# Optimization experiments

Hardware: AMD Instinct MI355X
Metric: run time of the kernel (lower is better)

## Reference

```python
import jax, jax.numpy as jnp
import numpy as np

B, N, C = 4, 8192, 128
NPOINT, NSAMPLE = 2048, 32
RADIUS = 0.1
EPS = 1e-5  # BatchNorm eps (eval mode with running stats)


def setup_inputs() -> dict:
    key = jax.random.key(0)
    k1, k2, k3 = jax.random.split(key, 3)
    return {
        "points_coor": jax.random.uniform(k1, (B, 3, N), dtype=jnp.float32),
        "points_fea": jax.random.normal(k2, (B, C, N), dtype=jnp.float32),
        "W": jax.random.normal(k3, (2 * C, C + 3), dtype=jnp.float32) * 0.05,
        "b": jnp.zeros((2 * C,), jnp.float32),
        "gamma": jnp.ones((2 * C,), jnp.float32),
        "beta": jnp.zeros((2 * C,), jnp.float32),
        "bn_mean": jnp.zeros((2 * C,), jnp.float32),
        "bn_var": jnp.ones((2 * C,), jnp.float32),
    }


def _fps_single(xyz):
    """Farthest point sampling for one cloud. xyz: (N,3) -> (NPOINT,) int32.
    Deterministic start at index 0 (torch version starts at a random index)."""
    n = xyz.shape[0]

    def body(carry, _):
        dist, farthest = carry
        centroid = xyz[farthest]                      # (3,)
        d = jnp.sum((xyz - centroid) ** 2, axis=-1)   # (N,)
        dist = jnp.minimum(dist, d)
        nxt = jnp.argmax(dist).astype(jnp.int32)
        return (dist, nxt), farthest

    init = (jnp.full((n,), 1e10, xyz.dtype), jnp.int32(0))
    (_, _), idx = jax.lax.scan(body, init, None, length=NPOINT)
    return idx


def _gather(points, idx):
    # points: (B,N,D), idx: (B,S,K) -> (B,S,K,D)
    return jax.vmap(lambda p, i: p[i])(points, idx)


def reference(points_coor, points_fea, W, b, gamma, beta, bn_mean, bn_var):
    coor = points_coor.transpose(0, 2, 1)  # (B,N,3)
    fea = points_fea.transpose(0, 2, 1)    # (B,N,C)

    # S: farthest point sampling
    fps_idx = jax.vmap(_fps_single)(coor)                              # (B,S)
    new_coor = jnp.take_along_axis(coor, fps_idx[:, :, None], axis=1)  # (B,S,3)

    # G: hybrid knn/ball query -- k nearest, out-of-radius replaced by nearest
    sq = (jnp.sum(new_coor ** 2, -1)[:, :, None]
          + jnp.sum(coor ** 2, -1)[:, None, :]
          - 2.0 * jnp.einsum('bsd,bnd->bsn', new_coor, coor))           # (B,S,N)
    neg_d, idx = jax.lax.top_k(-sq, NSAMPLE)                            # k smallest
    d = -neg_d
    group_idx = jnp.where(d > RADIUS ** 2, idx[:, :, 0:1], idx)         # (B,S,K)

    g_coor = (_gather(coor, group_idx) - new_coor[:, :, None, :]) / RADIUS  # (B,S,K,3)
    g_fea = _gather(fea, group_idx)                                         # (B,S,K,C)
    g = jnp.concatenate([g_fea, g_coor], axis=-1)                           # (B,S,K,C+3)

    # P: shared 1x1 conv + BN(eval) + ReLU, then max-pool over neighbors
    h = jnp.einsum('bskc,dc->bskd', g, W) + b
    h = gamma * (h - bn_mean) * jax.lax.rsqrt(bn_var + EPS) + beta
    h = jax.nn.relu(h)
    new_fea = jnp.max(h, axis=2)  # (B,S,2C)

    return new_coor.transpose(0, 2, 1), new_fea.transpose(0, 2, 1)
```

## Files before the change

kernel.cpp:

```cpp
#include <hip/hip_runtime.h>
#include <stdint.h>


typedef unsigned short u16;
typedef unsigned long long u64;
typedef __bf16 bf16x8 __attribute__((ext_vector_type(8)));
typedef float f32x4 __attribute__((ext_vector_type(4)));
typedef float f32x2 __attribute__((ext_vector_type(2)));

#define NB 4
#define NPTS 8192
#define CH 128
#define SPTS 2048
#define KN 32
#define CINP 160

__device__ __forceinline__ u16 f2b(float f) {
    unsigned x = __float_as_uint(f);
    unsigned r = (x + 0x7fffu + ((x >> 16) & 1u)) >> 16;
    return (u16)r;
}
__device__ __forceinline__ u64 umin64(u64 a, u64 b) { return a < b ? a : b; }

template <int CTRL>
__device__ __forceinline__ u64 dpp_max64(u64 k) {
    unsigned lo = (unsigned)k, hi = (unsigned)(k >> 32);
    unsigned mlo = (unsigned)__builtin_amdgcn_update_dpp((int)lo, (int)lo, CTRL, 0xF, 0xF, false);
    unsigned mhi = (unsigned)__builtin_amdgcn_update_dpp((int)hi, (int)hi, CTRL, 0xF, 0xF, false);
    u64 m = ((u64)mhi << 32) | mlo;
    return m > k ? m : k;
}
template <int CTRL>
__device__ __forceinline__ unsigned dpp_maxu(unsigned v) {
    unsigned mv = (unsigned)__builtin_amdgcn_update_dpp((int)v, (int)v, CTRL, 0xF, 0xF, false);
    return mv > v ? mv : v;
}

__global__ __launch_bounds__(256) void ktrans(const float* __restrict__ fea,
                                              u16* __restrict__ feaT) {
    __shared__ u16 T[128][130];
    int blk = blockIdx.x;
    int b = blk >> 6, nt = blk & 63;
    int n0 = nt * 128;
    int t = threadIdx.x;
#pragma unroll 4
    for (int it = 0; it < 64; ++it) {
        int idx = it * 256 + t;
        int c = idx >> 7, nl = idx & 127;
        T[nl][c] = f2b(fea[((size_t)(b * CH + c)) * NPTS + n0 + nl]);
    }
    __syncthreads();
#pragma unroll 4
    for (int it = 0; it < 64; ++it) {
        int idx = it * 256 + t;
        int nl = idx >> 7, c = idx & 127;
        feaT[((size_t)(b * NPTS + n0 + nl)) * CH + c] = T[nl][c];
    }
}

__global__ __launch_bounds__(256) void kmisc(const float* __restrict__ coor,
                                             const float* __restrict__ W,
                                             float* __restrict__ pp,
                                             u16* __restrict__ Wpad) {
    int gid = blockIdx.x * 256 + threadIdx.x;
    if (blockIdx.x < 128) {
        int n = gid & 8191, b = gid >> 13;
        const float* cb = coor + b * 3 * NPTS;
        float x = cb[n], y = cb[NPTS + n], z = cb[2 * NPTS + n];
        pp[gid] = __fadd_rn(__fadd_rn(__fmul_rn(x, x), __fmul_rn(y, y)),
                            __fmul_rn(z, z));
    } else {
        int i = gid - 128 * 256;
        if (i < 256 * CINP) {
            int d = i / CINP, k = i - d * CINP;
            Wpad[i] = (k < 131) ? f2b(W[d * 131 + k]) : (u16)0;
        }
    }
}

__global__ __launch_bounds__(256) void ksort(const float* __restrict__ coor,
                                             float* __restrict__ sxg,
                                             float* __restrict__ syg,
                                             float* __restrict__ szg,
                                             int* __restrict__ sog) {
    __shared__ int hist[16], base[16];
    int b = blockIdx.x, tid = threadIdx.x;
    const float* cb = coor + b * 3 * NPTS;
    if (tid < 16) hist[tid] = 0;
    __syncthreads();
    int bins[32];
#pragma unroll 4
    for (int i = 0; i < 32; ++i) {
        int n = tid * 32 + i;
        float x = cb[n], y = cb[NPTS + n];
        int bx = min(3, (int)(x * 4.0f));
        int by = min(3, (int)(y * 4.0f));
        int bin = by * 4 + bx;
        bins[i] = bin;
        atomicAdd(&hist[bin], 1);
    }
    __syncthreads();
    if (tid == 0) {
        int acc = 0;
        for (int k2 = 0; k2 < 16; ++k2) { base[k2] = acc; acc += hist[k2]; hist[k2] = 0; }
    }
    __syncthreads();
#pragma unroll 4
    for (int i = 0; i < 32; ++i) {
        int n = tid * 32 + i;
        int bin = bins[i];
        int pos = base[bin] + atomicAdd(&hist[bin], 1);
        sxg[b * NPTS + pos] = cb[n];
        syg[b * NPTS + pos] = cb[NPTS + n];
        szg[b * NPTS + pos] = cb[2 * NPTS + n];
        sog[b * NPTS + pos] = n;
    }
}

__global__ __launch_bounds__(1024) void kfps(const float* __restrict__ sxg,
                                             const float* __restrict__ syg,
                                             const float* __restrict__ szg,
                                             const int* __restrict__ sog,
                                             int* __restrict__ fpsIdx,
                                             float* __restrict__ outCoor) {
    __shared__ float4 sp[NPTS];
    __shared__ unsigned sWin[SPTS];
    __shared__ u64 sAtom[4];
    __shared__ int slot0s;
    int tid = threadIdx.x;
    int b = blockIdx.x;
    int lane = tid & 63;
    const float* gx = sxg + b * NPTS;
    const float* gy = syg + b * NPTS;
    const float* gz = szg + b * NPTS;
    const int* go = sog + b * NPTS;
    f32x2 X2[4], Y2[4], Z2[4], D2[4];
    unsigned PK[8];
    int n0 = tid * 8;
    if (tid < 4) sAtom[tid] = 0;
#pragma unroll
    for (int j = 0; j < 8; ++j) {
        float x = gx[n0 + j], y = gy[n0 + j], z = gz[n0 + j];
        sp[n0 + j] = make_float4(x, y, z, 0.0f);
        X2[j >> 1][j & 1] = x; Y2[j >> 1][j & 1] = y; Z2[j >> 1][j & 1] = z;
        D2[j >> 1][j & 1] = 1e10f;
        int oi = go[n0 + j];
        PK[j] = ((unsigned)oi << 16) | (unsigned)(n0 + j);
        if (oi == 0) slot0s = n0 + j;
    }
    float lox = X2[0][0], hix = lox, loy = Y2[0][0], hiy = loy, loz = Z2[0][0], hiz = loz;
#pragma unroll
    for (int j = 1; j < 8; ++j) {
        float x = X2[j >> 1][j & 1], y = Y2[j >> 1][j & 1], z = Z2[j >> 1][j & 1];
        lox = fminf(lox, x); hix = fmaxf(hix, x);
        loy = fminf(loy, y); hiy = fmaxf(hiy, y);
        loz = fminf(loz, z); hiz = fmaxf(hiz, z);
    }
#pragma unroll
    for (int off = 32; off > 0; off >>= 1) {
        lox = fminf(lox, __shfl_xor(lox, off)); hix = fmaxf(hix, __shfl_xor(hix, off));
        loy = fminf(loy, __shfl_xor(loy, off)); hiy = fmaxf(hiy, __shfl_xor(hiy, off));
        loz = fminf(loz, __shfl_xor(loz, off)); hiz = fmaxf(hiz, __shfl_xor(hiz, off));
    }
    __syncthreads();
    int far = slot0s;
    if (tid == 0) sWin[0] = (unsigned)slot0s;
    float wMaxF = 3.4e38f;
    u64 cachedKey = 1;
    for (int t = 1; t < SPTS; ++t) {
        float4 c = sp[far];
        float fx = c.x, fy = c.y, fz = c.z;
        float ddx = fmaxf(0.0f, fmaxf(lox - fx, fx - hix));
        float ddy = fmaxf(0.0f, fmaxf(loy - fy, fy - hiy));
        float ddz = fmaxf(0.0f, fmaxf(loz - fz, fz - hiz));
        float dmin2 = ddx * ddx + ddy * ddy + ddz * ddz;
        if (!(dmin2 * 0.9995f >= wMaxF)) {
            {
#pragma clang fp contract(off)
                f32x2 fx2 = {fx, fx}, fy2 = {fy, fy}, fz2 = {fz, fz};
#pragma unroll
                for (int i = 0; i < 4; ++i) {
                    f32x2 dx = X2[i] - fx2;
                    f32x2 dy = Y2[i] - fy2;
                    f32x2 dz = Z2[i] - fz2;
                    f32x2 s = (dx * dx + dy * dy) + dz * dz;
                    D2[i][0] = fminf(D2[i][0], s[0]);
                    D2[i][1] = fminf(D2[i][1], s[1]);
                }
            }
            float m01 = fmaxf(D2[0][0], D2[0][1]), m23 = fmaxf(D2[1][0], D2[1][1]);
            float m45 = fmaxf(D2[2][0], D2[2][1]), m67 = fmaxf(D2[3][0], D2[3][1]);
            float m = fmaxf(fmaxf(m01, m23), fmaxf(m45, m67));
            unsigned sel = 0xFFFFFFFFu;
#pragma unroll
            for (int j = 0; j < 8; ++j) {
                float dj = D2[j >> 1][j & 1];
                sel = (dj == m) ? (sel < PK[j] ? sel : PK[j]) : sel;
            }
            unsigned mbits = __float_as_uint(m);
            unsigned r = mbits;
            r = dpp_maxu<0xB1>(r);
            r = dpp_maxu<0x4E>(r);
            r = dpp_maxu<0x141>(r);
            r = dpp_maxu<0x140>(r);
            r = dpp_maxu<0x142>(r);
            r = dpp_maxu<0x143>(r);
            unsigned wmaxb = (unsigned)__builtin_amdgcn_readlane((int)r, 63);
            u64 ball = __ballot(mbits == wmaxb);
            unsigned wpk;
            if (__popcll(ball) == 1) {
                int l = __ffsll(ball) - 1;
                wpk = (unsigned)__builtin_amdgcn_readlane((int)sel, l);
            } else {
                u64 kk = (mbits == wmaxb) ? (((u64)wmaxb << 32) | (unsigned)~sel) : 0ull;
                kk = dpp_max64<0xB1>(kk);
                kk = dpp_max64<0x4E>(kk);
                kk = dpp_max64<0x141>(kk);
                kk = dpp_max64<0x140>(kk);
                kk = dpp_max64<0x142>(kk);
                kk = dpp_max64<0x143>(kk);
                unsigned lo = (unsigned)__builtin_amdgcn_readlane((int)(unsigned)kk, 63);
                wpk = ~lo;
            }
            cachedKey = ((u64)wmaxb << 32) | (unsigned)~wpk;
            wMaxF = __uint_as_float(wmaxb);
        }
        if (lane == 63) atomicMax(&sAtom[t & 3], cachedKey);
        if (tid == 0) sAtom[(t + 1) & 3] = 0;
        __syncthreads();
        u64 wk = sAtom[t & 3];
        unsigned pk = ~(unsigned)wk;
        far = (int)(pk & 0xFFFFu);
        if (tid == 0) sWin[t] = pk;
    }
    __syncthreads();
    for (int i = tid; i < SPTS; i += 1024) {
        unsigned pk = sWin[i];
        int slot = (int)(pk & 0xFFFFu);
        float4 c = sp[slot];
        fpsIdx[b * SPTS + i] = (int)(pk >> 16);
        float* oc = outCoor + b * 3 * SPTS + i;
        oc[0] = c.x; oc[SPTS] = c.y; oc[2 * SPTS] = c.z;
    }
}

__global__ __launch_bounds__(256) void kgroup(const float* __restrict__ coor,
                                              const float* __restrict__ pp,
                                              const int* __restrict__ fpsIdx,
                                              int* __restrict__ gidxOut) {
    __shared__ u64 buf[4][256];
    __shared__ int cnt[4];
    int tid = threadIdx.x;
    int wv = tid >> 6, lane = tid & 63;
    if (tid < 4) cnt[tid] = 0;
    __syncthreads();
    int row = blockIdx.x * 4 + wv;
    int b = row >> 11, s = row & 2047;
    const float* cb = coor + b * 3 * NPTS;
    int n0 = fpsIdx[b * SPTS + s];
    float cx = cb[n0], cy = cb[NPTS + n0], cz = cb[2 * NPTS + n0];
    float cc = __fadd_rn(__fadd_rn(__fmul_rn(cx, cx), __fmul_rn(cy, cy)),
                         __fmul_rn(cz, cz));
    const float* ppb = pp + b * NPTS;
    u64 mk = ~0ull;
    for (int n = lane; n < NPTS; n += 64) {
        float x = cb[n], y = cb[NPTS + n], z = cb[2 * NPTS + n];
        float dot = __fmaf_rn(cz, z, __fmaf_rn(cy, y, __fmul_rn(cx, x)));
        float sq = __fsub_rn(__fadd_rn(cc, ppb[n]), __fmul_rn(2.0f, dot));
        unsigned ub = __float_as_uint(sq);
        ub ^= (ub >> 31) ? 0xFFFFFFFFu : 0x80000000u;
        u64 key = ((u64)ub << 32) | (unsigned)n;
        mk = umin64(mk, key);
        if (sq <= 0.01f) {
            int p = atomicAdd(&cnt[wv], 1);
            if (p < 256) buf[wv][p] = key;
        }
    }
#pragma unroll
    for (int off = 32; off > 0; off >>= 1) mk = umin64(mk, __shfl_xor(mk, off));
    int C = cnt[wv];
    if (C > 256) C = 256;
    int* go = gidxOut + row * KN;
    if (C <= 32) {
        if (lane < 32) {
            unsigned idx = (lane < C) ? (unsigned)buf[wv][lane] : (unsigned)mk;
            go[lane] = (int)idx;
        }
    } else {
        u64 e[4];
#pragma unroll
        for (int i = 0; i < 4; ++i) {
            int j2 = lane + (i << 6);
            e[i] = (j2 < C) ? buf[wv][j2] : ~0ull;
        }
        int cl = 0;
        unsigned sel = 0;
        for (int it = 0; it < 32; ++it) {
            u64 lb = ~0ull;
            int li = 0;
#pragma unroll
            for (int i = 0; i < 4; ++i) {
                bool f = (((cl >> i) & 1) == 0) && (e[i] < lb);
                lb = f ? e[i] : lb;
                li = f ? i : li;
            }
            u64 wmin = lb;
#pragma unroll
            for (int off = 32; off > 0; off >>= 1) wmin = umin64(wmin, __shfl_xor(wmin, off));
            u64 bal = __ballot(lb == wmin);
            int src = __ffsll((unsigned long long)bal) - 1;
            if (lane == src) cl |= (1 << li);
            if (lane == it) sel = (unsigned)wmin;
        }
        if (lane < 32) go[lane] = (int)sel;
    }
}

__global__ __launch_bounds__(256) void kfeat(const float* __restrict__ coor,
                                             const u16* __restrict__ feaT,
                                             const u16* __restrict__ Wpad,
                                             const float* __restrict__ bias,
                                             const float* __restrict__ gamma,
                                             const float* __restrict__ beta,
                                             const float* __restrict__ bmean,
                                             const float* __restrict__ bvar,
                                             const int* __restrict__ fpsIdx,
                                             const int* __restrict__ gidx,
                                             float* __restrict__ outFea) {
    __shared__ u16 g[KN][168];
    int row = blockIdx.x;
    int b = row >> 11, s = row & 2047;
    int tid = threadIdx.x;
    {
        int k = tid >> 3, j = tid & 7;
        const float* cb = coor + b * 3 * NPTS;
        int nc = fpsIdx[b * SPTS + s];
        int nbr = gidx[row * KN + k];
        const uint4* f4 = (const uint4*)(feaT + (((size_t)b * NPTS + nbr) << 7));
        uint4* gr = (uint4*)&g[k][0];
        gr[j] = f4[j];
        gr[j + 8] = f4[j + 8];
        for (int c = 128 + j; c < CINP; c += 8) {
            u16 v = 0;
            if (c < 131) {
                int dim = c - 128;
                float pv = cb[dim * NPTS + nbr];
                float cv = cb[dim * NPTS + nc];
                v = f2b(__fdiv_rn(__fsub_rn(pv, cv), 0.1f));
            }
            g[k][c] = v;
        }
    }
    __syncthreads();
    int w = tid >> 6, lane = tid & 63;
    int mrow = lane & 15, q = lane >> 4;
    f32x4 acc[4][2] = {};
#pragma unroll
    for (int ks = 0; ks < 5; ++ks) {
        int kb = ks * 32 + q * 8;
        bf16x8 b0 = *(const bf16x8*)&g[mrow][kb];
        bf16x8 b1 = *(const bf16x8*)&g[mrow + 16][kb];
#pragma unroll
        for (int mt = 0; mt < 4; ++mt) {
            bf16x8 a = *(const bf16x8*)&Wpad[(size_t)(w * 64 + mt * 16 + mrow) * CINP + kb];
            acc[mt][0] = __builtin_amdgcn_mfma_f32_16x16x32_bf16(a, b0, acc[mt][0], 0, 0, 0);
            acc[mt][1] = __builtin_amdgcn_mfma_f32_16x16x32_bf16(a, b1, acc[mt][1], 0, 0, 0);
        }
    }
#pragma unroll
    for (int mt = 0; mt < 4; ++mt) {
#pragma unroll
        for (int r = 0; r < 4; ++r) {
            int m = w * 64 + mt * 16 + q * 4 + r;
            float ga = gamma[m], be = beta[m];
            float mu = bmean[m], va = bvar[m], bi = bias[m];
            float rs = 1.0f / sqrtf(va + 1e-5f);
            float h0 = acc[mt][0][r] + bi;
            h0 = fmaxf(ga * (h0 - mu) * rs + be, 0.0f);
            float h1 = acc[mt][1][r] + bi;
            h1 = fmaxf(ga * (h1 - mu) * rs + be, 0.0f);
            float v = fmaxf(h0, h1);
#pragma unroll
            for (int off = 1; off < 16; off <<= 1) v = fmaxf(v, __shfl_xor(v, off));
            if (mrow == 0) outFea[((size_t)(b * 256 + m)) * SPTS + s] = v;
        }
    }
}

extern "C" void kernel_launch(void* const* d_in, const int* in_sizes, int n_in,
                              void* d_out, int out_size, void* d_ws, size_t ws_size,
                              hipStream_t stream) {
    const float* coor = (const float*)d_in[0];
    const float* fea = (const float*)d_in[1];
    const float* W = (const float*)d_in[2];
    const float* bias = (const float*)d_in[3];
    const float* gamma = (const float*)d_in[4];
    const float* beta = (const float*)d_in[5];
    const float* bmean = (const float*)d_in[6];
    const float* bvar = (const float*)d_in[7];
    char* ws = (char*)d_ws;
    int* fpsIdx = (int*)ws;
    int* gidx = (int*)(ws + 32768);
    float* pp = (float*)(ws + 32768 + 1048576);
    u16* feaT = (u16*)(ws + 1212416);
    u16* Wpad = (u16*)(ws + 9601024);
    float* sxg = (float*)(ws + 9682944);
    float* syg = (float*)(ws + 9814016);
    float* szg = (float*)(ws + 9945088);
    int* sog = (int*)(ws + 10076160);
    float* outC = (float*)d_out;
    float* outF = outC + NB * 3 * SPTS;

    ktrans<<<256, 256, 0, stream>>>(fea, feaT);
    kmisc<<<288, 256, 0, stream>>>(coor, W, pp, Wpad);
    ksort<<<NB, 256, 0, stream>>>(coor, sxg, syg, szg, sog);
    kfps<<<NB, 1024, 0, stream>>>(sxg, syg, szg, sog, fpsIdx, outC);
    kgroup<<<2048, 256, 0, stream>>>(coor, pp, fpsIdx, gidx);
    kfeat<<<8192, 256, 0, stream>>>(coor, feaT, Wpad, bias, gamma, beta, bmean, bvar,
                                    fpsIdx, gidx, outF);
}
```

Before: 1.816 ms.

## Speculatively select two FPS points per iteration using top-2 reduction

The FPS loop now computes both the global maximum and runner-up distance keys per round, using two block-level atomic reductions. If the second candidate's distance to the first winner is no smaller than its current min-distance, the runner-up is provably the next farthest point, so two samples are committed in one iteration. This aims to cut the number of serial block-wide iterations and syncs in the 2048-step sequential loop. The cost is extra per-thread reduction work, a second barrier per iteration, and updating distances against two centroids.

```diff
diff --git a/kernel.cpp b/kernel.cpp
--- a/kernel.cpp
+++ b/kernel.cpp
@@ -21,6 +21,7 @@
     return (u16)r;
 }
 __device__ __forceinline__ u64 umin64(u64 a, u64 b) { return a < b ? a : b; }
+__device__ __forceinline__ u64 umax64(u64 a, u64 b) { return a > b ? a : b; }
 
 template <int CTRL>
 __device__ __forceinline__ u64 dpp_max64(u64 k) {
@@ -30,10 +31,16 @@
     u64 m = ((u64)mhi << 32) | mlo;
     return m > k ? m : k;
 }
-template <int CTRL>
-__device__ __forceinline__ unsigned dpp_maxu(unsigned v) {
-    unsigned mv = (unsigned)__builtin_amdgcn_update_dpp((int)v, (int)v, CTRL, 0xF, 0xF, false);
-    return mv > v ? mv : v;
+__device__ __forceinline__ u64 wave_max64(u64 k) {
+    k = dpp_max64<0xB1>(k);
+    k = dpp_max64<0x4E>(k);
+    k = dpp_max64<0x141>(k);
+    k = dpp_max64<0x140>(k);
+    k = dpp_max64<0x142>(k);
+    k = dpp_max64<0x143>(k);
+    unsigned lo = (unsigned)__builtin_amdgcn_readlane((int)(unsigned)k, 63);
+    unsigned hi = (unsigned)__builtin_amdgcn_readlane((int)(unsigned)(k >> 32), 63);
+    return ((u64)hi << 32) | lo;
 }
 
 __global__ __launch_bounds__(256) void ktrans(const float* __restrict__ fea,
@@ -125,19 +132,17 @@
                                              float* __restrict__ outCoor) {
     __shared__ float4 sp[NPTS];
     __shared__ unsigned sWin[SPTS];
-    __shared__ u64 sAtom[4];
+    __shared__ u64 sA[3], sB[3];
     __shared__ int slot0s;
-    int tid = threadIdx.x;
-    int b = blockIdx.x;
-    int lane = tid & 63;
+    int tid = threadIdx.x, b = blockIdx.x, lane = tid & 63;
     const float* gx = sxg + b * NPTS;
     const float* gy = syg + b * NPTS;
     const float* gz = szg + b * NPTS;
     const int* go = sog + b * NPTS;
     f32x2 X2[4], Y2[4], Z2[4], D2[4];
-    unsigned PK[8];
+    unsigned KLO[8];
     int n0 = tid * 8;
-    if (tid < 4) sAtom[tid] = 0;
+    if (tid < 3) { sA[tid] = 0; sB[tid] = 0; }
 #pragma unroll
     for (int j = 0; j < 8; ++j) {
         float x = gx[n0 + j], y = gy[n0 + j], z = gz[n0 + j];
@@ -145,7 +150,7 @@
         X2[j >> 1][j & 1] = x; Y2[j >> 1][j & 1] = y; Z2[j >> 1][j & 1] = z;
         D2[j >> 1][j & 1] = 1e10f;
         int oi = go[n0 + j];
-        PK[j] = ((unsigned)oi << 16) | (unsigned)(n0 + j);
+        KLO[j] = ~(((unsigned)oi << 16) | (unsigned)(n0 + j));
         if (oi == 0) slot0s = n0 + j;
     }
     float lox = X2[0][0], hix = lox, loy = Y2[0][0], hiy = loy, loz = Z2[0][0], hiz = loz;
@@ -163,75 +168,91 @@
         loz = fminf(loz, __shfl_xor(loz, off)); hiz = fmaxf(hiz, __shfl_xor(hiz, off));
     }
     __syncthreads();
-    int far = slot0s;
     if (tid == 0) sWin[0] = (unsigned)slot0s;
+    float4 c1 = sp[slot0s], c2 = c1;
+    int npend = 1, t = 1, r3 = 0;
     float wMaxF = 3.4e38f;
-    u64 cachedKey = 1;
-    for (int t = 1; t < SPTS; ++t) {
-        float4 c = sp[far];
-        float fx = c.x, fy = c.y, fz = c.z;
-        float ddx = fmaxf(0.0f, fmaxf(lox - fx, fx - hix));
-        float ddy = fmaxf(0.0f, fmaxf(loy - fy, fy - hiy));
-        float ddz = fmaxf(0.0f, fmaxf(loz - fz, fz - hiz));
-        float dmin2 = ddx * ddx + ddy * ddy + ddz * ddz;
-        if (!(dmin2 * 0.9995f >= wMaxF)) {
+    u64 cT1 = 1, cT2 = 0;
+    while (t < SPTS) {
+        float ex = fmaxf(fmaxf(lox - c1.x, c1.x - hix), 0.0f);
+        float ey = fmaxf(fmaxf(loy - c1.y, c1.y - hiy), 0.0f);
+        float ez = fmaxf(fmaxf(loz - c1.z, c1.z - hiz), 0.0f);
+        float dd = ex * ex + ey * ey + ez * ez;
+        if (npend == 2) {
+            float fx2_ = fmaxf(fmaxf(lox - c2.x, c2.x - hix), 0.0f);
+            float fy2_ = fmaxf(fmaxf(loy - c2.y, c2.y - hiy), 0.0f);
+            float fz2_ = fmaxf(fmaxf(loz - c2.z, c2.z - hiz), 0.0f);
+            dd = fminf(dd, fx2_ * fx2_ + fy2_ * fy2_ + fz2_ * fz2_);
+        }
+        if (!(dd * 0.9995f >= wMaxF)) {
             {
 #pragma clang fp contract(off)
-                f32x2 fx2 = {fx, fx}, fy2 = {fy, fy}, fz2 = {fz, fz};
+                f32x2 ax = {c1.x, c1.x}, ay = {c1.y, c1.y}, az = {c1.z, c1.z};
 #pragma unroll
                 for (int i = 0; i < 4; ++i) {
-                    f32x2 dx = X2[i] - fx2;
-                    f32x2 dy = Y2[i] - fy2;
-                    f32x2 dz = Z2[i] - fz2;
+                    f32x2 dx = X2[i] - ax, dy = Y2[i] - ay, dz = Z2[i] - az;
                     f32x2 s = (dx * dx + dy * dy) + dz * dz;
                     D2[i][0] = fminf(D2[i][0], s[0]);
                     D2[i][1] = fminf(D2[i][1], s[1]);
                 }
+                if (npend == 2) {
+                    f32x2 bx = {c2.x, c2.x}, by = {c2.y, c2.y}, bz = {c2.z, c2.z};
+#pragma unroll
+                    for (int i = 0; i < 4; ++i) {
+                        f32x2 dx = X2[i] - bx, dy = Y2[i] - by, dz = Z2[i] - bz;
+                        f32x2 s = (dx * dx + dy * dy) + dz * dz;
+                        D2[i][0] = fminf(D2[i][0], s[0]);
+                        D2[i][1] = fminf(D2[i][1], s[1]);
+                    }
+                }
             }
-            float m01 = fmaxf(D2[0][0], D2[0][1]), m23 = fmaxf(D2[1][0], D2[1][1]);
-            float m45 = fmaxf(D2[2][0], D2[2][1]), m67 = fmaxf(D2[3][0], D2[3][1]);
-            float m = fmaxf(fmaxf(m01, m23), fmaxf(m45, m67));
-            unsigned sel = 0xFFFFFFFFu;
+            u64 k[8];
+#pragma unroll
+            for (int j = 0; j < 8; ++j)
+                k[j] = ((u64)__float_as_uint(D2[j >> 1][j & 1]) << 32) | KLO[j];
+            u64 a01 = umax64(k[0], k[1]), a23 = umax64(k[2], k[3]);
+            u64 a45 = umax64(k[4], k[5]), a67 = umax64(k[6], k[7]);
+            u64 t1v = umax64(umax64(a01, a23), umax64(a45, a67));
+            u64 t2v = 0;
 #pragma unroll
             for (int j = 0; j < 8; ++j) {
-                float dj = D2[j >> 1][j & 1];
-                sel = (dj == m) ? (sel < PK[j] ? sel : PK[j]) : sel;
+                u64 kj = (k[j] == t1v) ? 0ull : k[j];
+                t2v = umax64(t2v, kj);
             }
-            unsigned mbits = __float_as_uint(m);
-            unsigned r = mbits;
-            r = dpp_maxu<0xB1>(r);
-            r = dpp_maxu<0x4E>(r);
-            r = dpp_maxu<0x141>(r);
-            r = dpp_maxu<0x140>(r);
-            r = dpp_maxu<0x142>(r);
-            r = dpp_maxu<0x143>(r);
-            unsigned wmaxb = (unsigned)__builtin_amdgcn_readlane((int)r, 63);
-            u64 ball = __ballot(mbits == wmaxb);
-            unsigned wpk;
-            if (__popcll(ball) == 1) {
-                int l = __ffsll(ball) - 1;
-                wpk = (unsigned)__builtin_amdgcn_readlane((int)sel, l);
-            } else {
-                u64 kk = (mbits == wmaxb) ? (((u64)wmaxb << 32) | (unsigned)~sel) : 0ull;
-                kk = dpp_max64<0xB1>(kk);
-                kk = dpp_max64<0x4E>(kk);
-                kk = dpp_max64<0x141>(kk);
-                kk = dpp_max64<0x140>(kk);
-                kk = dpp_max64<0x142>(kk);
-                kk = dpp_max64<0x143>(kk);
-                unsigned lo = (unsigned)__builtin_amdgcn_readlane((int)(unsigned)kk, 63);
-                wpk = ~lo;
-            }
-            cachedKey = ((u64)wmaxb << 32) | (unsigned)~wpk;
-            wMaxF = __uint_as_float(wmaxb);
-        }
-        if (lane == 63) atomicMax(&sAtom[t & 3], cachedKey);
-        if (tid == 0) sAtom[(t + 1) & 3] = 0;
+            u64 w1 = wave_max64(t1v);
+            u64 m2 = (t1v == w1) ? t2v : t1v;
+            u64 w2 = wave_max64(m2);
+            cT1 = w1; cT2 = w2;
+            wMaxF = __uint_as_float((unsigned)(w1 >> 32));
+        }
+        if (lane == 63) atomicMax(&sA[r3], cT1);
         __syncthreads();
-        u64 wk = sAtom[t & 3];
-        unsigned pk = ~(unsigned)wk;
-        far = (int)(pk & 0xFFFFu);
-        if (tid == 0) sWin[t] = pk;
+        u64 G1 = sA[r3];
+        unsigned pk1 = ~(unsigned)G1;
+        float4 n1 = sp[pk1 & 0xFFFFu];
+        u64 cand = (cT1 == G1) ? cT2 : cT1;
+        if (lane == 63) atomicMax(&sB[r3], cand);
+        if (tid == 0) {
+            int z = r3 + 2; if (z >= 3) z -= 3;
+            sA[z] = 0; sB[z] = 0;
+            sWin[t] = pk1;
+        }
+        __syncthreads();
+        u64 G2 = sB[r3];
+        unsigned pk2 = ~(unsigned)G2;
+        float4 n2 = sp[pk2 & 0xFFFFu];
+        float qx = __fsub_rn(n2.x, n1.x);
+        float qy = __fsub_rn(n2.y, n1.y);
+        float qz = __fsub_rn(n2.z, n1.z);
+        float dref = __fadd_rn(__fadd_rn(__fmul_rn(qx, qx), __fmul_rn(qy, qy)),
+                               __fmul_rn(qz, qz));
+        float Da2 = __uint_as_float((unsigned)(G2 >> 32));
+        bool two = (dref >= Da2) && (t + 1 < SPTS);
+        if (two && tid == 0) sWin[t + 1] = pk2;
+        c1 = n1; c2 = n2;
+        npend = two ? 2 : 1;
+        t += two ? 2 : 1;
+        r3 = (r3 == 2) ? 0 : r3 + 1;
     }
     __syncthreads();
     for (int i = tid; i < SPTS; i += 1024) {
```

Result: slower. 2.449 ms (+34.9%).
